# Kernel optimization log

Hardware: AMD Instinct MI355X
Metric: run time of the kernel (lower is better)

Reference implementation:

```python
import jax, jax.numpy as jnp
import numpy as np

D = 1024      # input_dim
H = 16        # head_num
HD = 64       # head_dim
HID = 4096    # mlp hidden
CUR = 512     # cur_seq
PREV = 512    # prev_seq (memory)
FULL = CUR + PREV
BS = 16
SCALE = 1.0 / (HD ** 0.5)


def setup_inputs() -> dict:
    key = jax.random.key(0)
    ks = jax.random.split(key, 20)
    def nrm(k, shape, s=0.02):
        return (jax.random.normal(k, shape) * s).astype(jnp.float32)
    inp = {
        "inputs": nrm(ks[0], (CUR, BS, D), 1.0),
        "pos_embedding": nrm(ks[1], (FULL, 1, D), 1.0),
        "u": nrm(ks[2], (H, HD)),
        "v": nrm(ks[3], (H, HD)),
        "memory": nrm(ks[4], (PREV, BS, D), 1.0),
        # causal mask: position i (query) may attend to j <= i + PREV; True = masked
        "mask": jnp.triu(jnp.ones((CUR, FULL), dtype=bool), k=PREV + 1)[:, :, None],
        # attention params (stored as (in, out); torch Linear applies x @ W.T + b)
        "Wkv": nrm(ks[5], (D, 2 * H * HD)), "bkv": jnp.zeros((2 * H * HD,), jnp.float32),
        "Wq": nrm(ks[6], (D, H * HD)), "bq": jnp.zeros((H * HD,), jnp.float32),
        "Wo": nrm(ks[7], (H * HD, D)), "bo": jnp.zeros((D,), jnp.float32),
        "Wp": nrm(ks[8], (D, H * HD)), "bp": jnp.zeros((H * HD,), jnp.float32),
        # layernorms
        "ln1_g": jnp.ones((D,), jnp.float32), "ln1_b": jnp.zeros((D,), jnp.float32),
        "ln2_g": jnp.ones((D,), jnp.float32), "ln2_b": jnp.zeros((D,), jnp.float32),
        # mlp (mlp_num=2): Linear(D,HID)+relu, Linear(HID,D)+relu
        "W1": nrm(ks[9], (D, HID)), "b1": jnp.zeros((HID,), jnp.float32),
        "W2": nrm(ks[10], (HID, D)), "b2": jnp.zeros((D,), jnp.float32),
        # GRU gates: stacked [Wr,Wz,Wg] and [Ur,Uz,Ug], no bias; bg init 2.0
        "g1_W": nrm(ks[11], (3, D, D)), "g1_U": nrm(ks[12], (3, D, D)),
        "g1_bg": jnp.full((D,), 2.0, jnp.float32),
        "g2_W": nrm(ks[13], (3, D, D)), "g2_U": nrm(ks[14], (3, D, D)),
        "g2_bg": jnp.full((D,), 2.0, jnp.float32),
    }
    return inp


def _layernorm(x, g, b, eps=1e-5):
    mu = jnp.mean(x, axis=-1, keepdims=True)
    var = jnp.mean(jnp.square(x - mu), axis=-1, keepdims=True)
    return (x - mu) * jax.lax.rsqrt(var + eps) * g + b


def _rel_shift(x):
    # x: (bs, head, cur, full) -> pad/reshape/slice trick of Transformer-XL
    b, h, c, f = x.shape
    xp = jnp.pad(x, ((0, 0), (0, 0), (0, 0), (1, 0)))      # (b,h,c,f+1)
    xp = xp.reshape(b, h, f + 1, c)
    return xp[:, :, 1:, :].reshape(b, h, c, f)


def _gru_gate(x, y, W, U, bg):
    # W, U: (3, D, D) for [r, z, g] gates; torch Linear => y @ W[i].T
    r = jax.nn.sigmoid(y @ W[0].T + x @ U[0].T)
    z = jax.nn.sigmoid(y @ W[1].T + x @ U[1].T - bg)
    h = jnp.tanh(y @ W[2].T + (r * x) @ U[2].T)
    return (1.0 - z) * x + z * h


def _attention_xl(x_cur, pos_emb, x_full, u, v, mask,
                  Wkv, bkv, Wq, bq, Wo, bo, Wp, bp):
    cur, bs, _ = x_cur.shape
    full = x_full.shape[0]
    kv = x_full @ Wkv + bkv                                  # (full, bs, 2*H*HD)
    key, value = jnp.split(kv, 2, axis=-1)
    query = x_cur @ Wq + bq                                  # (cur, bs, H*HD)
    r = (pos_emb @ Wp + bp).reshape(full, H, HD)             # (full, H, HD)

    key = key.reshape(full, bs, H, HD)
    value = value.reshape(full, bs, H, HD)
    query = query.reshape(cur, bs, H, HD)

    content = jnp.einsum('ibhd,jbhd->bhij', query + u, key)  # (bs,H,cur,full)
    position = jnp.einsum('ibhd,jhd->bhij', query + v, r)    # (bs,H,cur,full)
    position = _rel_shift(position)

    attn = (content + position) * SCALE
    # mask: (cur, full, 1) bool, True = masked
    m = mask[:, :, 0][None, None]                            # (1,1,cur,full)
    attn = jnp.where(m, -jnp.inf, attn)
    p = jax.nn.softmax(attn, axis=-1)

    out = jnp.einsum('bhij,jbhd->ibhd', p, value).reshape(cur, bs, H * HD)
    return out @ Wo + bo                                     # (cur, bs, D)


def reference(inputs, pos_embedding, u, v, memory, mask,
              Wkv, bkv, Wq, bq, Wo, bo, Wp, bp,
              ln1_g, ln1_b, ln2_g, ln2_b,
              W1, b1, W2, b2,
              g1_W, g1_U, g1_bg, g2_W, g2_U, g2_bg):
    prev = memory.shape[0]
    full_input = jnp.concatenate([memory, inputs], axis=0)   # (full, bs, D)
    x1 = _layernorm(full_input, ln1_g, ln1_b)
    a1 = _attention_xl(x1[prev:], pos_embedding, x1, u, v, mask,
                       Wkv, bkv, Wq, bq, Wo, bo, Wp, bp)
    a1 = jax.nn.relu(a1)                                     # dropout = identity (eval)
    o1 = _gru_gate(inputs, a1, g1_W, g1_U, g1_bg)
    x2 = _layernorm(o1, ln2_g, ln2_b)
    m2 = jax.nn.relu(jax.nn.relu(x2 @ W1 + b1) @ W2 + b2)    # mlp: act after every linear
    o2 = _gru_gate(o1, m2, g2_W, g2_U, g2_bg)
    return o2
```

## Files before the change

### kernel.cpp

```cpp
#include <hip/hip_runtime.h>
#include <stdint.h>

typedef _Float16 h16;
typedef __attribute__((ext_vector_type(8))) _Float16 f16x8;
typedef __attribute__((ext_vector_type(4))) _Float16 f16x4;
typedef __attribute__((ext_vector_type(4))) float f32x4;

enum { F_OBF = 1, F_BIAS = 2, F_RELU = 4, F_ACC = 8 };

#define BARRIER_MEM                                  \
  do {                                               \
    asm volatile("" ::: "memory");                   \
    __builtin_amdgcn_s_barrier();                    \
    asm volatile("" ::: "memory");                   \
  } while (0)

static __device__ __forceinline__ void gload16(const void* g, void* l) {
  __builtin_amdgcn_global_load_lds((__attribute__((address_space(1))) void*)g,
                                   (__attribute__((address_space(3))) void*)l,
                                   16, 0, 0);
}

template <int BN, int FLAGS>
__global__ __launch_bounds__(512) void gemm2_k(
    const h16* __restrict__ A, const h16* __restrict__ B,
    void* __restrict__ Cv, const float* __restrict__ bias,
    int K, int lda, int ldb, int ldc, int gm) {
  constexpr int NH = BN / 128;
  constexpr int WN = BN / 4;
  __shared__ h16 Al[2][256][64];
  __shared__ h16 Bl[2][BN][64];

  const int tid = threadIdx.x, lane = tid & 63, wid = tid >> 6;
  const int wr = wid >> 2, wn = wid & 3;
  const int ar = lane & 15, q4 = lane >> 4;

  const int nwg = gridDim.x, cpx = nwg >> 3;
  const int bid = (blockIdx.x & 7) * cpx + (blockIdx.x >> 3);
  const int mx = bid % gm, ny = bid / gm;

  const h16* Ab = A + (long)mx * 256 * lda;
  const h16* Bb = B + (long)ny * BN * ldb;

  auto stageA = [&](int buf, int half, int k0) {
#pragma unroll
    for (int l = 0; l < 2; ++l) {
      const int idx = l * 512 + tid;
      const int row = half * 128 + (idx >> 3), sl = idx & 7;
      gload16(Ab + (long)row * lda + k0 + (sl ^ (row & 7)) * 8,
              (char*)&Al[buf][0][0] + (half * 1024 + l * 512 + wid * 64) * 16);
    }
  };
  auto stageB = [&](int buf, int half, int k0) {
#pragma unroll
    for (int l = 0; l < NH; ++l) {
      const int idx = l * 512 + tid;
      const int row = half * (BN / 2) + (idx >> 3), sl = idx & 7;
      gload16(Bb + (long)row * ldb + k0 + (sl ^ (row & 7)) * 8,
              (char*)&Bl[buf][0][0] + (half * (BN * 4) + l * 512 + wid * 64) * 16);
    }
  };

  f32x4 acc[8][2 * NH] = {};
  const int nk = K >> 6;

  stageB(0, 0, 0); stageB(0, 1, 0); stageA(0, 0, 0); stageA(0, 1, 0);
  if (nk > 1) { stageB(1, 0, 64); stageB(1, 1, 64); stageA(1, 0, 64); stageA(1, 1, 64); }
  if (nk > 1) {
    if constexpr (NH == 2) asm volatile("s_waitcnt vmcnt(8)" ::: "memory");
    else                   asm volatile("s_waitcnt vmcnt(6)" ::: "memory");
  } else {
    asm volatile("s_waitcnt vmcnt(0)" ::: "memory");
  }
  BARRIER_MEM;

  for (int kt = 0; kt < nk; ++kt) {
    const int b = kt & 1;
    const int k2 = (kt + 2) << 6;
    const bool pf = (kt + 2) < nk;

    f16x8 a0[4][2], b0[NH][2];
#pragma unroll
    for (int m = 0; m < 4; ++m) {
      const int row = wr * 128 + m * 16 + ar;
#pragma unroll
      for (int ks = 0; ks < 2; ++ks)
        a0[m][ks] = *(const f16x8*)&Al[b][row][((ks * 4 + q4) ^ (row & 7)) * 8];
    }
#pragma unroll
    for (int n = 0; n < NH; ++n) {
      const int row = wn * WN + n * 16 + ar;
#pragma unroll
      for (int ks = 0; ks < 2; ++ks)
        b0[n][ks] = *(const f16x8*)&Bl[b][row][((ks * 4 + q4) ^ (row & 7)) * 8];
    }
    BARRIER_MEM;
    __builtin_amdgcn_s_setprio(1);
#pragma unroll
    for (int m = 0; m < 4; ++m)
#pragma unroll
      for (int n = 0; n < NH; ++n)
#pragma unroll
        for (int ks = 0; ks < 2; ++ks)
          acc[m][n] = __builtin_amdgcn_mfma_f32_16x16x32_f16(a0[m][ks], b0[n][ks], acc[m][n], 0, 0, 0);
    __builtin_amdgcn_s_setprio(0);
    BARRIER_MEM;

    f16x8 b1f[NH][2];
#pragma unroll
    for (int n = 0; n < NH; ++n) {
      const int row = wn * WN + (n + NH) * 16 + ar;
#pragma unroll
      for (int ks = 0; ks < 2; ++ks)
        b1f[n][ks] = *(const f16x8*)&Bl[b][row][((ks * 4 + q4) ^ (row & 7)) * 8];
    }
    BARRIER_MEM;
    __builtin_amdgcn_s_setprio(1);
#pragma unroll
    for (int m = 0; m < 4; ++m)
#pragma unroll
      for (int n = 0; n < NH; ++n)
#pragma unroll
        for (int ks = 0; ks < 2; ++ks)
          acc[m][n + NH] = __builtin_amdgcn_mfma_f32_16x16x32_f16(a0[m][ks], b1f[n][ks], acc[m][n + NH], 0, 0, 0);
    __builtin_amdgcn_s_setprio(0);
    BARRIER_MEM;

    f16x8 a1f[4][2];
#pragma unroll
    for (int m = 0; m < 4; ++m) {
      const int row = wr * 128 + (m + 4) * 16 + ar;
#pragma unroll
      for (int ks = 0; ks < 2; ++ks)
        a1f[m][ks] = *(const f16x8*)&Al[b][row][((ks * 4 + q4) ^ (row & 7)) * 8];
    }
    if (pf) { stageB(b, 0, k2); stageB(b, 1, k2); }
    BARRIER_MEM;
    __builtin_amdgcn_s_setprio(1);
#pragma unroll
    for (int m = 0; m < 4; ++m)
#pragma unroll
      for (int n = 0; n < NH; ++n)
#pragma unroll
        for (int ks = 0; ks < 2; ++ks)
          acc[m + 4][n] = __builtin_amdgcn_mfma_f32_16x16x32_f16(a1f[m][ks], b0[n][ks], acc[m + 4][n], 0, 0, 0);
    __builtin_amdgcn_s_setprio(0);
    BARRIER_MEM;

    if (pf) { stageA(b, 0, k2); stageA(b, 1, k2); }
    __builtin_amdgcn_s_setprio(1);
#pragma unroll
    for (int m = 0; m < 4; ++m)
#pragma unroll
      for (int n = 0; n < NH; ++n)
#pragma unroll
        for (int ks = 0; ks < 2; ++ks)
          acc[m + 4][n + NH] = __builtin_amdgcn_mfma_f32_16x16x32_f16(a1f[m][ks], b1f[n][ks], acc[m + 4][n + NH], 0, 0, 0);
    __builtin_amdgcn_s_setprio(0);
    if (pf) {
      if constexpr (NH == 2) asm volatile("s_waitcnt vmcnt(8)" ::: "memory");
      else                   asm volatile("s_waitcnt vmcnt(6)" ::: "memory");
    } else if (kt + 1 < nk) {
      asm volatile("s_waitcnt vmcnt(0)" ::: "memory");
    }
    BARRIER_MEM;
  }

#pragma unroll
  for (int m = 0; m < 8; ++m) {
#pragma unroll
    for (int n = 0; n < 2 * NH; ++n) {
      const int col = ny * BN + wn * WN + n * 16 + ar;
      float bv1 = 0.f;
      if (FLAGS & F_BIAS) bv1 = bias[col];
#pragma unroll
      for (int r = 0; r < 4; ++r) {
        const int row = mx * 256 + wr * 128 + m * 16 + q4 * 4 + r;
        float val = acc[m][n][r] + bv1;
        if (FLAGS & F_RELU) val = fmaxf(val, 0.f);
        if constexpr ((FLAGS & F_ACC) != 0) {
          float* p = (float*)Cv + (long)row * ldc + col;
          *p = *p + val;
        } else if constexpr ((FLAGS & F_OBF) != 0) {
          ((h16*)Cv)[(long)row * ldc + col] = (h16)val;
        } else {
          ((float*)Cv)[(long)row * ldc + col] = val;
        }
      }
    }
  }
}

__global__ __launch_bounds__(256) void fattn_k(
    const h16* __restrict__ qu, const h16* __restrict__ qv,
    const h16* __restrict__ kvb, const h16* __restrict__ vT,
    const h16* __restrict__ rb, h16* __restrict__ attn) {
  __shared__ h16 Kl[2][128][64];
  __shared__ h16 Vl[64][128];
  __shared__ h16 Psc[4][16][164];

  const int tid = threadIdx.x, lane = tid & 63, wv = tid >> 6;
  const int z = blockIdx.x, b = z >> 4, h = z & 15;
  const int i0 = blockIdx.y * 64;
  const int ar = lane & 15, q4 = lane >> 4;
  const int myrow = i0 + wv * 16;
  const h16* vTz = vT + (long)z * 64 * 1024;

  const long qoff = ((long)(myrow + ar) * 16 + b) * 1024 + h * 64 + q4 * 8;
  f16x8 quf[2], qvf[2];
  quf[0] = *(const f16x8*)&qu[qoff];
  quf[1] = *(const f16x8*)&qu[qoff + 32];
  qvf[0] = *(const f16x8*)&qv[qoff];
  qvf[1] = *(const f16x8*)&qv[qoff + 32];

  f32x4 o[4] = {};
  float mrow[4], lrow[4];
#pragma unroll
  for (int r = 0; r < 4; ++r) { mrow[r] = -3e38f; lrow[r] = 0.f; }

  const int ntiles = (i0 + 575 + 128) >> 7;

  auto stageK = [&](int buf, int j0) {
#pragma unroll
    for (int it = 0; it < 4; ++it) {
      const int ch = it * 256 + wv * 64 + lane;
      const int kr = ch >> 3, ks = ch & 7;
      gload16(kvb + ((long)(j0 + kr) * 16 + b) * 2048 + h * 64 + (ks ^ (kr & 7)) * 8,
              (char*)&Kl[buf][0][0] + (it * 256 + wv * 64) * 16);
    }
  };
  auto stageV = [&](int j0) {
#pragma unroll
    for (int it = 0; it < 4; ++it) {
      const int ch = it * 256 + wv * 64 + lane;
      const int vd = ch >> 4, vs = ch & 15;
      gload16(vTz + (long)vd * 1024 + j0 + (vs ^ (vd & 7)) * 8,
              (char*)&Vl[0][0] + (it * 256 + wv * 64) * 16);
    }
  };

  stageK(0, 0);
  asm volatile("s_waitcnt vmcnt(0)" ::: "memory");
  __builtin_amdgcn_s_barrier();

  for (int t = 0; t < ntiles; ++t) {
    const int j0 = t * 128;
    const int kb = t & 1;
    const bool pk = (t + 1) < ntiles;

    stageV(j0);
    if (pk) stageK(kb ^ 1, (t + 1) * 128);
    if (pk) asm volatile("s_waitcnt vmcnt(8)" ::: "memory");
    else    asm volatile("s_waitcnt vmcnt(4)" ::: "memory");
    BARRIER_MEM;

    f32x4 acc_c[8] = {};
#pragma unroll
    for (int kd = 0; kd < 2; ++kd)
#pragma unroll
      for (int nf = 0; nf < 8; ++nf) {
        const int j = nf * 16 + ar;
        const int phys = (kd * 4 + q4) ^ (j & 7);
        const f16x8 kf = *(const f16x8*)&Kl[kb][j][phys * 8];
        acc_c[nf] = __builtin_amdgcn_mfma_f32_16x16x32_f16(quf[kd], kf, acc_c[nf], 0, 0, 0);
      }

    const int jbase = j0 - myrow + 496;
    f32x4 acc_p[9] = {};
#pragma unroll
    for (int kd = 0; kd < 2; ++kd)
#pragma unroll
      for (int jf = 0; jf < 9; ++jf) {
        int jjr = jbase + jf * 16 + ar;
        if (jjr > 1023) jjr = 1023;
        const f16x8 rf = *(const f16x8*)&rb[(long)jjr * 1024 + h * 64 + kd * 32 + q4 * 8];
        acc_p[jf] = __builtin_amdgcn_mfma_f32_16x16x32_f16(qvf[kd], rf, acc_p[jf], 0, 0, 0);
      }
#pragma unroll
    for (int jf = 0; jf < 9; ++jf)
#pragma unroll
      for (int r = 0; r < 4; ++r)
        Psc[wv][q4 * 4 + r][jf * 16 + ar] = (h16)acc_p[jf][r];

    float p[8][4];
#pragma unroll
    for (int nf = 0; nf < 8; ++nf)
#pragma unroll
      for (int r = 0; r < 4; ++r) {
        const int iloc = q4 * 4 + r;
        const int jloc = nf * 16 + ar;
        const int band = jloc - iloc + 15;
        const float pv = (float)Psc[wv][iloc][band];
        float sv = (acc_c[nf][r] + pv) * 0.125f;
        const bool ok = (j0 + jloc) <= (myrow + iloc + 512);
        p[nf][r] = ok ? sv : -3e38f;
      }
#pragma unroll
    for (int r = 0; r < 4; ++r) {
      float tm = -3e38f;
#pragma unroll
      for (int nf = 0; nf < 8; ++nf) tm = fmaxf(tm, p[nf][r]);
      tm = fmaxf(tm, __shfl_xor(tm, 1));
      tm = fmaxf(tm, __shfl_xor(tm, 2));
      tm = fmaxf(tm, __shfl_xor(tm, 4));
      tm = fmaxf(tm, __shfl_xor(tm, 8));
      const float mn = fmaxf(mrow[r], tm);
      const float sc = __expf(mrow[r] - mn);
      mrow[r] = mn;
      float ts = 0.f;
#pragma unroll
      for (int nf = 0; nf < 8; ++nf) {
        const float e = __expf(p[nf][r] - mn);
        p[nf][r] = e;
        ts += e;
      }
      ts += __shfl_xor(ts, 1);
      ts += __shfl_xor(ts, 2);
      ts += __shfl_xor(ts, 4);
      ts += __shfl_xor(ts, 8);
      lrow[r] = lrow[r] * sc + ts;
#pragma unroll
      for (int v = 0; v < 4; ++v) o[v][r] *= sc;
    }

#pragma unroll
    for (int nf = 0; nf < 8; ++nf)
#pragma unroll
      for (int r = 0; r < 4; ++r) {
        const int iloc = q4 * 4 + r, jloc = nf * 16 + ar;
        Psc[wv][iloc][((jloc >> 3) ^ (iloc & 7)) * 8 + (jloc & 7)] = (h16)p[nf][r];
      }

    if (pk) asm volatile("s_waitcnt vmcnt(4)" ::: "memory");
    else    asm volatile("s_waitcnt vmcnt(0)" ::: "memory");
    BARRIER_MEM;

#pragma unroll
    for (int ks = 0; ks < 4; ++ks) {
      const f16x8 pa = *(const f16x8*)&Psc[wv][ar][((ks * 4 + q4) ^ (ar & 7)) * 8];
#pragma unroll
      for (int vnf = 0; vnf < 4; ++vnf) {
        const int d = vnf * 16 + ar;
        const f16x8 vb = *(const f16x8*)&Vl[d][((ks * 4 + q4) ^ (d & 7)) * 8];
        o[vnf] = __builtin_amdgcn_mfma_f32_16x16x32_f16(pa, vb, o[vnf], 0, 0, 0);
      }
    }
    BARRIER_MEM;
  }

#pragma unroll
  for (int vnf = 0; vnf < 4; ++vnf)
#pragma unroll
    for (int r = 0; r < 4; ++r) {
      const int i_ = myrow + q4 * 4 + r;
      attn[((long)i_ * 16 + b) * 1024 + h * 64 + vnf * 16 + ar] =
          (h16)(o[vnf][r] / lrow[r]);
    }
}

__global__ __launch_bounds__(256) void wtrans_k(const float* __restrict__ in,
                                                h16* __restrict__ out, int K, int N) {
  __shared__ float t[32][33];
  const int tx = threadIdx.x & 31, ty = threadIdx.x >> 5;
  const int n0 = blockIdx.x * 32, k0 = blockIdx.y * 32;
#pragma unroll
  for (int j = 0; j < 32; j += 8)
    t[ty + j][tx] = in[(long)(k0 + ty + j) * N + n0 + tx];
  __syncthreads();
#pragma unroll
  for (int j = 0; j < 32; j += 8)
    out[(long)(n0 + ty + j) * K + k0 + tx] = (h16)t[tx][ty + j];
}

__global__ __launch_bounds__(256) void cast_k(const float* __restrict__ in,
                                              h16* __restrict__ out, long n4) {
  const long i = (long)blockIdx.x * 256 + threadIdx.x;
  if (i >= n4) return;
  const float4 v = ((const float4*)in)[i];
  f16x4 o;
  o[0] = (h16)v.x; o[1] = (h16)v.y; o[2] = (h16)v.z; o[3] = (h16)v.w;
  ((f16x4*)out)[i] = o;
}

__global__ __launch_bounds__(256) void cast4_k(
    const float* __restrict__ a, const float* __restrict__ b,
    const float* __restrict__ c, const float* __restrict__ d,
    h16* __restrict__ oa, h16* __restrict__ ob,
    h16* __restrict__ oc, h16* __restrict__ od, long n4) {
  const long i = (long)blockIdx.x * 256 + threadIdx.x;
  if (i >= n4) return;
  const float* in = (blockIdx.y == 0) ? a : (blockIdx.y == 1) ? b : (blockIdx.y == 2) ? c : d;
  h16* out = (blockIdx.y == 0) ? oa : (blockIdx.y == 1) ? ob : (blockIdx.y == 2) ? oc : od;
  const float4 v = ((const float4*)in)[i];
  f16x4 o;
  o[0] = (h16)v.x; o[1] = (h16)v.y; o[2] = (h16)v.z; o[3] = (h16)v.w;
  ((f16x4*)out)[i] = o;
}

__global__ void addbias_k(const float* __restrict__ bq, const float* __restrict__ u,
                          const float* __restrict__ v, float* __restrict__ qu,
                          float* __restrict__ qv) {
  const int c = blockIdx.x * 256 + threadIdx.x;
  if (c < 1024) { qu[c] = bq[c] + u[c]; qv[c] = bq[c] + v[c]; }
}

__global__ __launch_bounds__(256) void zero_out_k(float* __restrict__ out, long n) {
  const long i = (long)blockIdx.x * 256 + threadIdx.x;
  if (i < n) out[i] = 0.f;
}

__global__ __launch_bounds__(256) void ln_k(const float* __restrict__ src0,
                                            const float* __restrict__ src1, int rows0,
                                            const float* __restrict__ g,
                                            const float* __restrict__ b,
                                            h16* __restrict__ out) {
  const int row = blockIdx.x, tid = threadIdx.x;
  const float* src = (row < rows0) ? (src0 + (long)row * 1024)
                                   : (src1 + (long)(row - rows0) * 1024);
  const float4 x = ((const float4*)src)[tid];
  float s = x.x + x.y + x.z + x.w;
  float sq = x.x * x.x + x.y * x.y + x.z * x.z + x.w * x.w;
#pragma unroll
  for (int o = 32; o > 0; o >>= 1) { s += __shfl_down(s, o); sq += __shfl_down(sq, o); }
  __shared__ float red[8];
  const int lane = tid & 63, w = tid >> 6;
  if (lane == 0) { red[w] = s; red[4 + w] = sq; }
  __syncthreads();
  s = red[0] + red[1] + red[2] + red[3];
  sq = red[4] + red[5] + red[6] + red[7];
  const float mu = s * (1.f / 1024.f);
  const float inv = rsqrtf(sq * (1.f / 1024.f) - mu * mu + 1e-5f);
  const float4 gg = ((const float4*)g)[tid], bb = ((const float4*)b)[tid];
  f16x4 o;
  o[0] = (h16)((x.x - mu) * inv * gg.x + bb.x);
  o[1] = (h16)((x.y - mu) * inv * gg.y + bb.y);
  o[2] = (h16)((x.z - mu) * inv * gg.z + bb.z);
  o[3] = (h16)((x.w - mu) * inv * gg.w + bb.w);
  ((f16x4*)(out + (long)row * 1024))[tid] = o;
}

__global__ __launch_bounds__(256) void vtrans_k(const h16* __restrict__ kv,
                                                h16* __restrict__ vT) {
  const int z = blockIdx.y, b = z >> 4, h = z & 15;
  const int j0 = blockIdx.x * 64;
  __shared__ h16 t[64][72];
  const int jj = threadIdx.x >> 3, c = threadIdx.x & 7;
#pragma unroll
  for (int half = 0; half < 2; ++half) {
    const int j = jj + half * 32;
    const f16x8 v = *(const f16x8*)(kv + ((long)(j0 + j) * 16 + b) * 2048 + 1024 + h * 64 + c * 8);
    *(f16x8*)&t[j][c * 8] = v;
  }
  __syncthreads();
#pragma unroll
  for (int half = 0; half < 2; ++half) {
    const int d = jj + half * 32;
    f16x8 o;
#pragma unroll
    for (int k = 0; k < 8; ++k) o[k] = t[c * 8 + k][d];
    *(f16x8*)(vT + ((long)z * 64 + d) * 1024 + j0 + c * 8) = o;
  }
}

__global__ __launch_bounds__(256) void gru_rx_k(const float* __restrict__ T,
                                                const float* __restrict__ x,
                                                h16* __restrict__ rx) {
  const long i = (long)blockIdx.x * 256 + threadIdx.x;
  const long row = i >> 8;
  const int c4 = (int)(i & 255);
  const float4 t = *((const float4*)(T + row * 3072) + c4);
  const float4 xx = ((const float4*)x)[i];
  f16x4 o;
  o[0] = (h16)(xx.x / (1.f + __expf(-t.x)));
  o[1] = (h16)(xx.y / (1.f + __expf(-t.y)));
  o[2] = (h16)(xx.z / (1.f + __expf(-t.z)));
  o[3] = (h16)(xx.w / (1.f + __expf(-t.w)));
  ((f16x4*)rx)[i] = o;
}

__global__ __launch_bounds__(256) void gru_out_k(const float* __restrict__ T,
                                                 const float* __restrict__ x,
                                                 const float* __restrict__ bg,
                                                 float* __restrict__ outf,
                                                 h16* __restrict__ outh) {
  const long i = (long)blockIdx.x * 256 + threadIdx.x;
  const long row = i >> 8;
  const int c4 = (int)(i & 255);
  const float4 tz = *((const float4*)(T + row * 3072 + 1024) + c4);
  const float4 th = *((const float4*)(T + row * 3072 + 2048) + c4);
  const float4 xx = ((const float4*)x)[i];
  const float4 bb = ((const float4*)bg)[c4];
  float4 o;
  {
    const float z0 = 1.f / (1.f + __expf(-(tz.x - bb.x)));
    const float z1 = 1.f / (1.f + __expf(-(tz.y - bb.y)));
    const float z2 = 1.f / (1.f + __expf(-(tz.z - bb.z)));
    const float z3 = 1.f / (1.f + __expf(-(tz.w - bb.w)));
    o.x = (1.f - z0) * xx.x + z0 * tanhf(th.x);
    o.y = (1.f - z1) * xx.y + z1 * tanhf(th.y);
    o.z = (1.f - z2) * xx.z + z2 * tanhf(th.z);
    o.w = (1.f - z3) * xx.w + z3 * tanhf(th.w);
  }
  ((float4*)outf)[i] = o;
  if (outh != nullptr) {
    f16x4 oh;
    oh[0] = (h16)o.x; oh[1] = (h16)o.y; oh[2] = (h16)o.z; oh[3] = (h16)o.w;
    ((f16x4*)outh)[i] = oh;
  }
}

extern "C" void kernel_launch(void* const* d_in, const int* in_sizes, int n_in,
                              void* d_out, int out_size, void* d_ws, size_t ws_size,
                              hipStream_t stream) {
  const float* inputs = (const float*)d_in[0];
  const float* pos    = (const float*)d_in[1];
  const float* u      = (const float*)d_in[2];
  const float* v      = (const float*)d_in[3];
  const float* memory = (const float*)d_in[4];
  const float* Wkv = (const float*)d_in[6];  const float* bkv = (const float*)d_in[7];
  const float* Wq  = (const float*)d_in[8];  const float* bq  = (const float*)d_in[9];
  const float* Wo  = (const float*)d_in[10]; const float* bo  = (const float*)d_in[11];
  const float* Wp  = (const float*)d_in[12]; const float* bp  = (const float*)d_in[13];
  const float* ln1_g = (const float*)d_in[14]; const float* ln1_b = (const float*)d_in[15];
  const float* ln2_g = (const float*)d_in[16]; const float* ln2_b = (const float*)d_in[17];
  const float* W1 = (const float*)d_in[18]; const float* b1 = (const float*)d_in[19];
  const float* W2 = (const float*)d_in[20]; const float* b2 = (const float*)d_in[21];
  const float* g1_W = (const float*)d_in[22]; const float* g1_U = (const float*)d_in[23];
  const float* g1_bg = (const float*)d_in[24];
  const float* g2_W = (const float*)d_in[25]; const float* g2_U = (const float*)d_in[26];
  const float* g2_bg = (const float*)d_in[27];
  (void)in_sizes; (void)n_in;

  const size_t MB = 1u << 20;
  const size_t NEEDED = 247 * MB;
  const dim3 blk(256);
  if (ws_size < NEEDED) {
    zero_out_k<<<(out_size + 255) / 256, blk, 0, stream>>>((float*)d_out, out_size);
    return;
  }

  char* w = (char*)d_ws;
  h16* WoT   = (h16*)(w + 0 * MB);
  h16* W1T   = (h16*)(w + 2 * MB);
  h16* W2T   = (h16*)(w + 10 * MB);
  h16* g1Wb  = (h16*)(w + 18 * MB);
  h16* g1Ub  = (h16*)(w + 24 * MB);
  h16* g2Wb  = (h16*)(w + 30 * MB);
  h16* g2Ub  = (h16*)(w + 36 * MB);
  h16* WkvT  = (h16*)(w + 42 * MB);
  h16* WqT   = (h16*)(w + 46 * MB);
  h16* WpT   = (h16*)(w + 48 * MB);
  h16* posb  = (h16*)(w + 50 * MB);
  float* bias_qu = (float*)(w + 52 * MB);
  float* bias_qv = (float*)(w + 52 * MB + 8192);
  h16* xb    = (h16*)(w + 53 * MB);
  h16* x1    = (h16*)(w + 69 * MB);
  char* Rbig =        w + 101 * MB;
  h16* qu    = (h16*)(w + 197 * MB);
  h16* qv    = (h16*)(w + 213 * MB);
  h16* rb    = (h16*)(w + 229 * MB);
  h16* attn  = (h16*)(w + 231 * MB);

  h16*   kvb  = (h16*)Rbig;
  float* Tall = (float*)Rbig;
  h16*   h1   = (h16*)Rbig;
  h16*   vT   = x1;
  h16*   a1   = qu;
  h16*   rx1  = qv;
  float* o1f  = (float*)qu;
  h16*   o1b  = attn;
  h16*   x2   = x1;
  h16*   m2   = x1 + 8L * 1024 * 1024;
  h16*   rx2  = x1;

  wtrans_k<<<dim3(64, 32), blk, 0, stream>>>(Wkv, WkvT, 1024, 2048);
  wtrans_k<<<dim3(32, 32), blk, 0, stream>>>(Wq, WqT, 1024, 1024);
  wtrans_k<<<dim3(32, 32), blk, 0, stream>>>(Wo, WoT, 1024, 1024);
  wtrans_k<<<dim3(32, 32), blk, 0, stream>>>(Wp, WpT, 1024, 1024);
  wtrans_k<<<dim3(128, 32), blk, 0, stream>>>(W1, W1T, 1024, 4096);
  wtrans_k<<<dim3(32, 128), blk, 0, stream>>>(W2, W2T, 4096, 1024);
  cast4_k<<<dim3(3072, 4), blk, 0, stream>>>(g1_W, g1_U, g2_W, g2_U,
                                             g1Wb, g1Ub, g2Wb, g2Ub, 786432);
  cast_k<<<1024, blk, 0, stream>>>(pos, posb, 262144);
  cast_k<<<8192, blk, 0, stream>>>(inputs, xb, 2097152);
  addbias_k<<<4, blk, 0, stream>>>(bq, u, v, bias_qu, bias_qv);

  ln_k<<<16384, blk, 0, stream>>>(memory, inputs, 8192, ln1_g, ln1_b, x1);

  gemm2_k<256, F_OBF | F_BIAS><<<dim3(512), dim3(512), 0, stream>>>(
      x1, WkvT, kvb, bkv, 1024, 1024, 1024, 2048, 64);
  gemm2_k<128, F_OBF | F_BIAS><<<dim3(256), dim3(512), 0, stream>>>(
      x1 + 8192L * 1024, WqT, qu, bias_qu, 1024, 1024, 1024, 1024, 32);
  gemm2_k<128, F_OBF | F_BIAS><<<dim3(256), dim3(512), 0, stream>>>(
      x1 + 8192L * 1024, WqT, qv, bias_qv, 1024, 1024, 1024, 1024, 32);
  gemm2_k<128, F_OBF | F_BIAS><<<dim3(32), dim3(512), 0, stream>>>(
      posb, WpT, rb, bp, 1024, 1024, 1024, 1024, 4);
  vtrans_k<<<dim3(16, 256), blk, 0, stream>>>(kvb, vT);

  fattn_k<<<dim3(256, 8), blk, 0, stream>>>(qu, qv, kvb, vT, rb, attn);

  gemm2_k<128, F_OBF | F_BIAS | F_RELU><<<dim3(256), dim3(512), 0, stream>>>(
      attn, WoT, a1, bo, 1024, 1024, 1024, 1024, 32);

  gemm2_k<256, 0><<<dim3(384), dim3(512), 0, stream>>>(
      a1, g1Wb, Tall, nullptr, 1024, 1024, 1024, 3072, 32);
  gemm2_k<256, F_ACC><<<dim3(256), dim3(512), 0, stream>>>(
      xb, g1Ub, Tall, nullptr, 1024, 1024, 1024, 3072, 32);
  gru_rx_k<<<8192, blk, 0, stream>>>(Tall, inputs, rx1);
  gemm2_k<128, F_ACC><<<dim3(256), dim3(512), 0, stream>>>(
      rx1, g1Ub + 2L * 1024 * 1024, Tall + 2048, nullptr, 1024, 1024, 1024, 3072, 32);
  gru_out_k<<<8192, blk, 0, stream>>>(Tall, inputs, g1_bg, o1f, o1b);

  ln_k<<<8192, blk, 0, stream>>>(o1f, o1f, 8192, ln2_g, ln2_b, x2);
  gemm2_k<256, F_OBF | F_BIAS | F_RELU><<<dim3(512), dim3(512), 0, stream>>>(
      x2, W1T, h1, b1, 1024, 1024, 1024, 4096, 32);
  gemm2_k<128, F_OBF | F_BIAS | F_RELU><<<dim3(256), dim3(512), 0, stream>>>(
      h1, W2T, m2, b2, 4096, 4096, 4096, 1024, 32);

  gemm2_k<256, 0><<<dim3(384), dim3(512), 0, stream>>>(
      m2, g2Wb, Tall, nullptr, 1024, 1024, 1024, 3072, 32);
  gemm2_k<256, F_ACC><<<dim3(256), dim3(512), 0, stream>>>(
      o1b, g2Ub, Tall, nullptr, 1024, 1024, 1024, 3072, 32);
  gru_rx_k<<<8192, blk, 0, stream>>>(Tall, o1f, rx2);
  gemm2_k<128, F_ACC><<<dim3(256), dim3(512), 0, stream>>>(
      rx2, g2Ub + 2L * 1024 * 1024, Tall + 2048, nullptr, 1024, 1024, 1024, 3072, 32);
  gru_out_k<<<8192, blk, 0, stream>>>(Tall, o1f, g2_bg, (float*)d_out, nullptr);
}
```

Before: 1.118 ms.

## Fuse qu/qv projections and restructure attention relative-position shift via shuffles

The two query GEMMs that differ only in bias are merged into one GEMM with a dual-output epilogue, so the activation and weight traffic for Wq is read once. In the attention kernel, the relative-shift band extraction now goes through cross-lane shuffles instead of a shared-memory round trip. The K tile drops to a single buffer with a rescheduled barrier/prefetch order, and positional-embedding loads are issued early. Single-buffering K shrinks LDS use but serialises some K loads against compute, and the added shuffles raise register pressure.

```diff
diff --git a/kernel.cpp b/kernel.cpp
--- a/kernel.cpp
+++ b/kernel.cpp
@@ -6,7 +6,7 @@
 typedef __attribute__((ext_vector_type(4))) _Float16 f16x4;
 typedef __attribute__((ext_vector_type(4))) float f32x4;
 
-enum { F_OBF = 1, F_BIAS = 2, F_RELU = 4, F_ACC = 8 };
+enum { F_OBF = 1, F_BIAS = 2, F_RELU = 4, F_ACC = 8, F_DUAL = 16 };
 
 #define BARRIER_MEM                                  \
   do {                                               \
@@ -25,7 +25,8 @@
 __global__ __launch_bounds__(512) void gemm2_k(
     const h16* __restrict__ A, const h16* __restrict__ B,
     void* __restrict__ Cv, const float* __restrict__ bias,
-    int K, int lda, int ldb, int ldc, int gm) {
+    int K, int lda, int ldb, int ldc, int gm,
+    void* __restrict__ C2v, const float* __restrict__ bias2) {
   constexpr int NH = BN / 128;
   constexpr int WN = BN / 4;
   __shared__ h16 Al[2][256][64];
@@ -171,8 +172,9 @@
 #pragma unroll
     for (int n = 0; n < 2 * NH; ++n) {
       const int col = ny * BN + wn * WN + n * 16 + ar;
-      float bv1 = 0.f;
+      float bv1 = 0.f, bv2 = 0.f;
       if (FLAGS & F_BIAS) bv1 = bias[col];
+      if (FLAGS & F_DUAL) bv2 = bias2[col];
 #pragma unroll
       for (int r = 0; r < 4; ++r) {
         const int row = mx * 256 + wr * 128 + m * 16 + q4 * 4 + r;
@@ -183,6 +185,8 @@
           *p = *p + val;
         } else if constexpr ((FLAGS & F_OBF) != 0) {
           ((h16*)Cv)[(long)row * ldc + col] = (h16)val;
+          if constexpr ((FLAGS & F_DUAL) != 0)
+            ((h16*)C2v)[(long)row * ldc + col] = (h16)(acc[m][n][r] + bv2);
         } else {
           ((float*)Cv)[(long)row * ldc + col] = val;
         }
@@ -191,13 +195,13 @@
   }
 }
 
-__global__ __launch_bounds__(256) void fattn_k(
+__global__ __launch_bounds__(256, 1) void fattn_k(
     const h16* __restrict__ qu, const h16* __restrict__ qv,
     const h16* __restrict__ kvb, const h16* __restrict__ vT,
     const h16* __restrict__ rb, h16* __restrict__ attn) {
-  __shared__ h16 Kl[2][128][64];
+  __shared__ h16 Kl[128][64];
   __shared__ h16 Vl[64][128];
-  __shared__ h16 Psc[4][16][164];
+  __shared__ h16 Psc[4][16][128];
 
   const int tid = threadIdx.x, lane = tid & 63, wv = tid >> 6;
   const int z = blockIdx.x, b = z >> 4, h = z & 15;
@@ -220,13 +224,13 @@
 
   const int ntiles = (i0 + 575 + 128) >> 7;
 
-  auto stageK = [&](int buf, int j0) {
+  auto stageK = [&](int j0) {
 #pragma unroll
     for (int it = 0; it < 4; ++it) {
       const int ch = it * 256 + wv * 64 + lane;
       const int kr = ch >> 3, ks = ch & 7;
       gload16(kvb + ((long)(j0 + kr) * 16 + b) * 2048 + h * 64 + (ks ^ (kr & 7)) * 8,
-              (char*)&Kl[buf][0][0] + (it * 256 + wv * 64) * 16);
+              (char*)&Kl[0][0] + (it * 256 + wv * 64) * 16);
     }
   };
   auto stageV = [&](int j0) {
@@ -239,20 +243,23 @@
     }
   };
 
-  stageK(0, 0);
-  asm volatile("s_waitcnt vmcnt(0)" ::: "memory");
-  __builtin_amdgcn_s_barrier();
+  stageK(0);
 
   for (int t = 0; t < ntiles; ++t) {
     const int j0 = t * 128;
-    const int kb = t & 1;
     const bool pk = (t + 1) < ntiles;
 
-    stageV(j0);
-    if (pk) stageK(kb ^ 1, (t + 1) * 128);
-    if (pk) asm volatile("s_waitcnt vmcnt(8)" ::: "memory");
-    else    asm volatile("s_waitcnt vmcnt(4)" ::: "memory");
-    BARRIER_MEM;
+    asm volatile("s_waitcnt vmcnt(0)" ::: "memory");
+    BARRIER_MEM;
+
+    const int jbase = j0 - myrow + 496;
+    f16x8 rf0[9];
+#pragma unroll
+    for (int jf = 0; jf < 9; ++jf) {
+      int jjr = jbase + jf * 16 + ar;
+      if (jjr > 1023) jjr = 1023;
+      rf0[jf] = *(const f16x8*)&rb[(long)jjr * 1024 + h * 64 + q4 * 8];
+    }
 
     f32x4 acc_c[8] = {};
 #pragma unroll
@@ -261,40 +268,47 @@
       for (int nf = 0; nf < 8; ++nf) {
         const int j = nf * 16 + ar;
         const int phys = (kd * 4 + q4) ^ (j & 7);
-        const f16x8 kf = *(const f16x8*)&Kl[kb][j][phys * 8];
+        const f16x8 kf = *(const f16x8*)&Kl[j][phys * 8];
         acc_c[nf] = __builtin_amdgcn_mfma_f32_16x16x32_f16(quf[kd], kf, acc_c[nf], 0, 0, 0);
       }
-
-    const int jbase = j0 - myrow + 496;
+    BARRIER_MEM;
+
+    f16x8 rf1[9];
+#pragma unroll
+    for (int jf = 0; jf < 9; ++jf) {
+      int jjr = jbase + jf * 16 + ar;
+      if (jjr > 1023) jjr = 1023;
+      rf1[jf] = *(const f16x8*)&rb[(long)jjr * 1024 + h * 64 + 32 + q4 * 8];
+    }
+    stageV(j0);
+    if (pk) stageK((t + 1) * 128);
+
     f32x4 acc_p[9] = {};
 #pragma unroll
-    for (int kd = 0; kd < 2; ++kd)
-#pragma unroll
-      for (int jf = 0; jf < 9; ++jf) {
-        int jjr = jbase + jf * 16 + ar;
-        if (jjr > 1023) jjr = 1023;
-        const f16x8 rf = *(const f16x8*)&rb[(long)jjr * 1024 + h * 64 + kd * 32 + q4 * 8];
-        acc_p[jf] = __builtin_amdgcn_mfma_f32_16x16x32_f16(qvf[kd], rf, acc_p[jf], 0, 0, 0);
+    for (int jf = 0; jf < 9; ++jf)
+      acc_p[jf] = __builtin_amdgcn_mfma_f32_16x16x32_f16(qvf[0], rf0[jf], acc_p[jf], 0, 0, 0);
+#pragma unroll
+    for (int jf = 0; jf < 9; ++jf)
+      acc_p[jf] = __builtin_amdgcn_mfma_f32_16x16x32_f16(qvf[1], rf1[jf], acc_p[jf], 0, 0, 0);
+
+    float p[8][4];
+#pragma unroll
+    for (int r = 0; r < 4; ++r) {
+      const int iloc = q4 * 4 + r;
+      const int src = q4 * 16 + ((ar - iloc + 15) & 15);
+      float g[9];
+#pragma unroll
+      for (int jf = 0; jf < 9; ++jf) g[jf] = __shfl(acc_p[jf][r], src, 64);
+      const bool hi = ar > iloc;
+      const int lim = myrow + iloc + 512 - j0;
+#pragma unroll
+      for (int nf = 0; nf < 8; ++nf) {
+        const float pv = hi ? g[nf + 1] : g[nf];
+        const float sv = (acc_c[nf][r] + pv) * 0.125f;
+        p[nf][r] = (nf * 16 + ar <= lim) ? sv : -3e38f;
       }
-#pragma unroll
-    for (int jf = 0; jf < 9; ++jf)
-#pragma unroll
-      for (int r = 0; r < 4; ++r)
-        Psc[wv][q4 * 4 + r][jf * 16 + ar] = (h16)acc_p[jf][r];
-
-    float p[8][4];
-#pragma unroll
-    for (int nf = 0; nf < 8; ++nf)
-#pragma unroll
-      for (int r = 0; r < 4; ++r) {
-        const int iloc = q4 * 4 + r;
-        const int jloc = nf * 16 + ar;
-        const int band = jloc - iloc + 15;
-        const float pv = (float)Psc[wv][iloc][band];
-        float sv = (acc_c[nf][r] + pv) * 0.125f;
-        const bool ok = (j0 + jloc) <= (myrow + iloc + 512);
-        p[nf][r] = ok ? sv : -3e38f;
-      }
+    }
+
 #pragma unroll
     for (int r = 0; r < 4; ++r) {
       float tm = -3e38f;
@@ -345,7 +359,6 @@
         o[vnf] = __builtin_amdgcn_mfma_f32_16x16x32_f16(pa, vb, o[vnf], 0, 0, 0);
       }
     }
-    BARRIER_MEM;
   }
 
 #pragma unroll
@@ -588,41 +601,41 @@
   ln_k<<<16384, blk, 0, stream>>>(memory, inputs, 8192, ln1_g, ln1_b, x1);
 
   gemm2_k<256, F_OBF | F_BIAS><<<dim3(512), dim3(512), 0, stream>>>(
-      x1, WkvT, kvb, bkv, 1024, 1024, 1024, 2048, 64);
-  gemm2_k<128, F_OBF | F_BIAS><<<dim3(256), dim3(512), 0, stream>>>(
-      x1 + 8192L * 1024, WqT, qu, bias_qu, 1024, 1024, 1024, 1024, 32);
-  gemm2_k<128, F_OBF | F_BIAS><<<dim3(256), dim3(512), 0, stream>>>(
-      x1 + 8192L * 1024, WqT, qv, bias_qv, 1024, 1024, 1024, 1024, 32);
+      x1, WkvT, kvb, bkv, 1024, 1024, 1024, 2048, 64, nullptr, nullptr);
+  gemm2_k<128, F_OBF | F_BIAS | F_DUAL><<<dim3(256), dim3(512), 0, stream>>>(
+      x1 + 8192L * 1024, WqT, qu, bias_qu, 1024, 1024, 1024, 1024, 32, qv, bias_qv);
   gemm2_k<128, F_OBF | F_BIAS><<<dim3(32), dim3(512), 0, stream>>>(
-      posb, WpT, rb, bp, 1024, 1024, 1024, 1024, 4);
+      posb, WpT, rb, bp, 1024, 1024, 1024, 1024, 4, nullptr, nullptr);
   vtrans_k<<<dim3(16, 256), blk, 0, stream>>>(kvb, vT);
 
   fattn_k<<<dim3(256, 8), blk, 0, stream>>>(qu, qv, kvb, vT, rb, attn);
 
   gemm2_k<128, F_OBF | F_BIAS | F_RELU><<<dim3(256), dim3(512), 0, stream>>>(
-      attn, WoT, a1, bo, 1024, 1024, 1024, 1024, 32);
+      attn, WoT, a1, bo, 1024, 1024, 1024, 1024, 32, nullptr, nullptr);
 
   gemm2_k<256, 0><<<dim3(384), dim3(512), 0, stream>>>(
-      a1, g1Wb, Tall, nullptr, 1024, 1024, 1024, 3072, 32);
+      a1, g1Wb, Tall, nullptr, 1024, 1024, 1024, 3072, 32, nullptr, nullptr);
   gemm2_k<256, F_ACC><<<dim3(256), dim3(512), 0, stream>>>(
-      xb, g1Ub, Tall, nullptr, 1024, 1024, 1024, 3072, 32);
+      xb, g1Ub, Tall, nullptr, 1024, 1024, 1024, 3072, 32, nullptr, nullptr);
   gru_rx_k<<<8192, blk, 0, stream>>>(Tall, inputs, rx1);
   gemm2_k<128, F_ACC><<<dim3(256), dim3(512), 0, stream>>>(
-      rx1, g1Ub + 2L * 1024 * 1024, Tall + 2048, nullptr, 1024, 1024, 1024, 3072, 32);
+      rx1, g1Ub + 2L * 1024 * 1024, Tall + 2048, nullptr, 1024, 1024, 1024, 3072, 32,
+      nullptr, nullptr);
   gru_out_k<<<8192, blk, 0, stream>>>(Tall, inputs, g1_bg, o1f, o1b);
 
   ln_k<<<8192, blk, 0, stream>>>(o1f, o1f, 8192, ln2_g, ln2_b, x2);
   gemm2_k<256, F_OBF | F_BIAS | F_RELU><<<dim3(512), dim3(512), 0, stream>>>(
-      x2, W1T, h1, b1, 1024, 1024, 1024, 4096, 32);
+      x2, W1T, h1, b1, 1024, 1024, 1024, 4096, 32, nullptr, nullptr);
   gemm2_k<128, F_OBF | F_BIAS | F_RELU><<<dim3(256), dim3(512), 0, stream>>>(
-      h1, W2T, m2, b2, 4096, 4096, 4096, 1024, 32);
+      h1, W2T, m2, b2, 4096, 4096, 4096, 1024, 32, nullptr, nullptr);
 
   gemm2_k<256, 0><<<dim3(384), dim3(512), 0, stream>>>(
-      m2, g2Wb, Tall, nullptr, 1024, 1024, 1024, 3072, 32);
+      m2, g2Wb, Tall, nullptr, 1024, 1024, 1024, 3072, 32, nullptr, nullptr);
   gemm2_k<256, F_ACC><<<dim3(256), dim3(512), 0, stream>>>(
-      o1b, g2Ub, Tall, nullptr, 1024, 1024, 1024, 3072, 32);
+      o1b, g2Ub, Tall, nullptr, 1024, 1024, 1024, 3072, 32, nullptr, nullptr);
   gru_rx_k<<<8192, blk, 0, stream>>>(Tall, o1f, rx2);
   gemm2_k<128, F_ACC><<<dim3(256), dim3(512), 0, stream>>>(
-      rx2, g2Ub + 2L * 1024 * 1024, Tall + 2048, nullptr, 1024, 1024, 1024, 3072, 32);
+      rx2, g2Ub + 2L * 1024 * 1024, Tall + 2048, nullptr, 1024, 1024, 1024, 3072, 32,
+      nullptr, nullptr);
   gru_out_k<<<8192, blk, 0, stream>>>(Tall, o1f, g2_bg, (float*)d_out, nullptr);
 }
```

Measured after the change: 1.215 ms. 8.7% more time.

## Concatenate GRU W/U weights into K=2048 GEMMs and fuse dual Q projections

Applied to the files above, without the earlier changes.

Packs each GRU gate's W and U matrices side by side into one K=2048 weight, and writes the activation and the gate input interleaved into a [y|x] buffer. Each gate stage then runs as a single longer-K GEMM instead of separate GEMMs plus read-modify-write accumulation into an fp32 buffer. The two Q projections (with u and v biases) now share one GEMM that writes two outputs. This removes redundant launches, accumulation traffic and a repeated Q GEMM, at the cost of a more intricate buffer layout and aliasing.

```diff
diff --git a/kernel.cpp b/kernel.cpp
--- a/kernel.cpp
+++ b/kernel.cpp
@@ -6,7 +6,7 @@
 typedef __attribute__((ext_vector_type(4))) _Float16 f16x4;
 typedef __attribute__((ext_vector_type(4))) float f32x4;
 
-enum { F_OBF = 1, F_BIAS = 2, F_RELU = 4, F_ACC = 8 };
+enum { F_OBF = 1, F_BIAS = 2, F_RELU = 4, F_ACC = 8, F_DUAL = 16 };
 
 #define BARRIER_MEM                                  \
   do {                                               \
@@ -25,7 +25,8 @@
 __global__ __launch_bounds__(512) void gemm2_k(
     const h16* __restrict__ A, const h16* __restrict__ B,
     void* __restrict__ Cv, const float* __restrict__ bias,
-    int K, int lda, int ldb, int ldc, int gm) {
+    int K, int lda, int ldb, int ldc, int gm,
+    void* __restrict__ C2v, const float* __restrict__ bias2) {
   constexpr int NH = BN / 128;
   constexpr int WN = BN / 4;
   __shared__ h16 Al[2][256][64];
@@ -171,8 +172,9 @@
 #pragma unroll
     for (int n = 0; n < 2 * NH; ++n) {
       const int col = ny * BN + wn * WN + n * 16 + ar;
-      float bv1 = 0.f;
+      float bv1 = 0.f, bv2 = 0.f;
       if (FLAGS & F_BIAS) bv1 = bias[col];
+      if (FLAGS & F_DUAL) bv2 = bias2[col];
 #pragma unroll
       for (int r = 0; r < 4; ++r) {
         const int row = mx * 256 + wr * 128 + m * 16 + q4 * 4 + r;
@@ -183,6 +185,8 @@
           *p = *p + val;
         } else if constexpr ((FLAGS & F_OBF) != 0) {
           ((h16*)Cv)[(long)row * ldc + col] = (h16)val;
+          if constexpr ((FLAGS & F_DUAL) != 0)
+            ((h16*)C2v)[(long)row * ldc + col] = (h16)(acc[m][n][r] + bv2);
         } else {
           ((float*)Cv)[(long)row * ldc + col] = val;
         }
@@ -382,19 +386,36 @@
   ((f16x4*)out)[i] = o;
 }
 
-__global__ __launch_bounds__(256) void cast4_k(
-    const float* __restrict__ a, const float* __restrict__ b,
-    const float* __restrict__ c, const float* __restrict__ d,
-    h16* __restrict__ oa, h16* __restrict__ ob,
-    h16* __restrict__ oc, h16* __restrict__ od, long n4) {
+__global__ __launch_bounds__(256) void gateprep_k(
+    const float* __restrict__ W1g, const float* __restrict__ U1g,
+    const float* __restrict__ W2g, const float* __restrict__ U2g,
+    h16* __restrict__ o1, h16* __restrict__ o2) {
   const long i = (long)blockIdx.x * 256 + threadIdx.x;
-  if (i >= n4) return;
-  const float* in = (blockIdx.y == 0) ? a : (blockIdx.y == 1) ? b : (blockIdx.y == 2) ? c : d;
-  h16* out = (blockIdx.y == 0) ? oa : (blockIdx.y == 1) ? ob : (blockIdx.y == 2) ? oc : od;
+  const long elem = i * 4;
+  const int row = (int)(elem >> 11);
+  const int col = (int)(elem & 2047);
+  const int gate = row >> 10, oc = row & 1023;
+  const float* W = (blockIdx.y == 0) ? W1g : W2g;
+  const float* U = (blockIdx.y == 0) ? U1g : U2g;
+  h16* out = (blockIdx.y == 0) ? o1 : o2;
+  const float* src = (col < 1024)
+      ? (W + (long)gate * 1048576 + (long)oc * 1024 + col)
+      : (U + (long)gate * 1048576 + (long)oc * 1024 + (col - 1024));
+  const float4 v = *(const float4*)src;
+  f16x4 o;
+  o[0] = (h16)v.x; o[1] = (h16)v.y; o[2] = (h16)v.z; o[3] = (h16)v.w;
+  *(f16x4*)(out + elem) = o;
+}
+
+__global__ __launch_bounds__(256) void xcast_k(const float* __restrict__ in,
+                                               h16* __restrict__ yx) {
+  const long i = (long)blockIdx.x * 256 + threadIdx.x;
+  const long row = i >> 8;
+  const int c4 = (int)(i & 255);
   const float4 v = ((const float4*)in)[i];
   f16x4 o;
   o[0] = (h16)v.x; o[1] = (h16)v.y; o[2] = (h16)v.z; o[3] = (h16)v.w;
-  ((f16x4*)out)[i] = o;
+  *(f16x4*)(yx + row * 2048 + 1024 + c4 * 4) = o;
 }
 
 __global__ void addbias_k(const float* __restrict__ bq, const float* __restrict__ u,
@@ -464,21 +485,22 @@
 
 __global__ __launch_bounds__(256) void gru_rx_k(const float* __restrict__ T,
                                                 const float* __restrict__ x,
-                                                h16* __restrict__ rx) {
+                                                h16* __restrict__ yx) {
   const long i = (long)blockIdx.x * 256 + threadIdx.x;
   const long row = i >> 8;
   const int c4 = (int)(i & 255);
-  const float4 t = *((const float4*)(T + row * 3072) + c4);
+  const float4 t = *((const float4*)(T + row * 2048) + c4);
   const float4 xx = ((const float4*)x)[i];
   f16x4 o;
   o[0] = (h16)(xx.x / (1.f + __expf(-t.x)));
   o[1] = (h16)(xx.y / (1.f + __expf(-t.y)));
   o[2] = (h16)(xx.z / (1.f + __expf(-t.z)));
   o[3] = (h16)(xx.w / (1.f + __expf(-t.w)));
-  ((f16x4*)rx)[i] = o;
+  *(f16x4*)(yx + row * 2048 + 1024 + c4 * 4) = o;
 }
 
 __global__ __launch_bounds__(256) void gru_out_k(const float* __restrict__ T,
+                                                 const float* __restrict__ G,
                                                  const float* __restrict__ x,
                                                  const float* __restrict__ bg,
                                                  float* __restrict__ outf,
@@ -486,8 +508,8 @@
   const long i = (long)blockIdx.x * 256 + threadIdx.x;
   const long row = i >> 8;
   const int c4 = (int)(i & 255);
-  const float4 tz = *((const float4*)(T + row * 3072 + 1024) + c4);
-  const float4 th = *((const float4*)(T + row * 3072 + 2048) + c4);
+  const float4 tz = *((const float4*)(T + row * 2048 + 1024) + c4);
+  const float4 th = *((const float4*)(G + row * 1024) + c4);
   const float4 xx = ((const float4*)x)[i];
   const float4 bb = ((const float4*)bg)[c4];
   float4 o;
@@ -505,7 +527,7 @@
   if (outh != nullptr) {
     f16x4 oh;
     oh[0] = (h16)o.x; oh[1] = (h16)o.y; oh[2] = (h16)o.z; oh[3] = (h16)o.w;
-    ((f16x4*)outh)[i] = oh;
+    *(f16x4*)(outh + row * 2048 + 1024 + c4 * 4) = oh;
   }
 }
 
@@ -543,35 +565,30 @@
   h16* WoT   = (h16*)(w + 0 * MB);
   h16* W1T   = (h16*)(w + 2 * MB);
   h16* W2T   = (h16*)(w + 10 * MB);
-  h16* g1Wb  = (h16*)(w + 18 * MB);
-  h16* g1Ub  = (h16*)(w + 24 * MB);
-  h16* g2Wb  = (h16*)(w + 30 * MB);
-  h16* g2Ub  = (h16*)(w + 36 * MB);
+  h16* g1B   = (h16*)(w + 18 * MB);
+  h16* g2B   = (h16*)(w + 30 * MB);
   h16* WkvT  = (h16*)(w + 42 * MB);
   h16* WqT   = (h16*)(w + 46 * MB);
   h16* WpT   = (h16*)(w + 48 * MB);
   h16* posb  = (h16*)(w + 50 * MB);
   float* bias_qu = (float*)(w + 52 * MB);
   float* bias_qv = (float*)(w + 52 * MB + 8192);
-  h16* xb    = (h16*)(w + 53 * MB);
-  h16* x1    = (h16*)(w + 69 * MB);
-  char* Rbig =        w + 101 * MB;
-  h16* qu    = (h16*)(w + 197 * MB);
-  h16* qv    = (h16*)(w + 213 * MB);
-  h16* rb    = (h16*)(w + 229 * MB);
-  h16* attn  = (h16*)(w + 231 * MB);
+  h16* yx1   = (h16*)(w + 53 * MB);
+  h16* x1    = (h16*)(w + 85 * MB);
+  char* Rbig =        w + 117 * MB;
+  h16* qu    = (h16*)(w + 181 * MB);
+  h16* qv    = (h16*)(w + 197 * MB);
+  h16* attn  = (h16*)(w + 213 * MB);
+  h16* rb    = (h16*)(w + 245 * MB);
 
   h16*   kvb  = (h16*)Rbig;
-  float* Tall = (float*)Rbig;
+  float* Trz  = (float*)Rbig;
   h16*   h1   = (h16*)Rbig;
+  float* Tg   = (float*)qu;
   h16*   vT   = x1;
-  h16*   a1   = qu;
-  h16*   rx1  = qv;
-  float* o1f  = (float*)qu;
-  h16*   o1b  = attn;
-  h16*   x2   = x1;
-  h16*   m2   = x1 + 8L * 1024 * 1024;
-  h16*   rx2  = x1;
+  h16*   yx2  = x1;
+  float* o1f  = (float*)attn;
+  h16*   x2   = yx1;
 
   wtrans_k<<<dim3(64, 32), blk, 0, stream>>>(Wkv, WkvT, 1024, 2048);
   wtrans_k<<<dim3(32, 32), blk, 0, stream>>>(Wq, WqT, 1024, 1024);
@@ -579,50 +596,43 @@
   wtrans_k<<<dim3(32, 32), blk, 0, stream>>>(Wp, WpT, 1024, 1024);
   wtrans_k<<<dim3(128, 32), blk, 0, stream>>>(W1, W1T, 1024, 4096);
   wtrans_k<<<dim3(32, 128), blk, 0, stream>>>(W2, W2T, 4096, 1024);
-  cast4_k<<<dim3(3072, 4), blk, 0, stream>>>(g1_W, g1_U, g2_W, g2_U,
-                                             g1Wb, g1Ub, g2Wb, g2Ub, 786432);
+  gateprep_k<<<dim3(6144, 2), blk, 0, stream>>>(g1_W, g1_U, g2_W, g2_U, g1B, g2B);
   cast_k<<<1024, blk, 0, stream>>>(pos, posb, 262144);
-  cast_k<<<8192, blk, 0, stream>>>(inputs, xb, 2097152);
+  xcast_k<<<8192, blk, 0, stream>>>(inputs, yx1);
   addbias_k<<<4, blk, 0, stream>>>(bq, u, v, bias_qu, bias_qv);
 
   ln_k<<<16384, blk, 0, stream>>>(memory, inputs, 8192, ln1_g, ln1_b, x1);
 
   gemm2_k<256, F_OBF | F_BIAS><<<dim3(512), dim3(512), 0, stream>>>(
-      x1, WkvT, kvb, bkv, 1024, 1024, 1024, 2048, 64);
-  gemm2_k<128, F_OBF | F_BIAS><<<dim3(256), dim3(512), 0, stream>>>(
-      x1 + 8192L * 1024, WqT, qu, bias_qu, 1024, 1024, 1024, 1024, 32);
-  gemm2_k<128, F_OBF | F_BIAS><<<dim3(256), dim3(512), 0, stream>>>(
-      x1 + 8192L * 1024, WqT, qv, bias_qv, 1024, 1024, 1024, 1024, 32);
+      x1, WkvT, kvb, bkv, 1024, 1024, 1024, 2048, 64, nullptr, nullptr);
+  gemm2_k<128, F_OBF | F_BIAS | F_DUAL><<<dim3(256), dim3(512), 0, stream>>>(
+      x1 + 8192L * 1024, WqT, qu, bias_qu, 1024, 1024, 1024, 1024, 32, qv, bias_qv);
   gemm2_k<128, F_OBF | F_BIAS><<<dim3(32), dim3(512), 0, stream>>>(
-      posb, WpT, rb, bp, 1024, 1024, 1024, 1024, 4);
+      posb, WpT, rb, bp, 1024, 1024, 1024, 1024, 4, nullptr, nullptr);
   vtrans_k<<<dim3(16, 256), blk, 0, stream>>>(kvb, vT);
 
   fattn_k<<<dim3(256, 8), blk, 0, stream>>>(qu, qv, kvb, vT, rb, attn);
 
   gemm2_k<128, F_OBF | F_BIAS | F_RELU><<<dim3(256), dim3(512), 0, stream>>>(
-      attn, WoT, a1, bo, 1024, 1024, 1024, 1024, 32);
-
-  gemm2_k<256, 0><<<dim3(384), dim3(512), 0, stream>>>(
-      a1, g1Wb, Tall, nullptr, 1024, 1024, 1024, 3072, 32);
-  gemm2_k<256, F_ACC><<<dim3(256), dim3(512), 0, stream>>>(
-      xb, g1Ub, Tall, nullptr, 1024, 1024, 1024, 3072, 32);
-  gru_rx_k<<<8192, blk, 0, stream>>>(Tall, inputs, rx1);
-  gemm2_k<128, F_ACC><<<dim3(256), dim3(512), 0, stream>>>(
-      rx1, g1Ub + 2L * 1024 * 1024, Tall + 2048, nullptr, 1024, 1024, 1024, 3072, 32);
-  gru_out_k<<<8192, blk, 0, stream>>>(Tall, inputs, g1_bg, o1f, o1b);
+      attn, WoT, yx1, bo, 1024, 1024, 1024, 2048, 32, nullptr, nullptr);
+
+  gemm2_k<256, 0><<<dim3(256), dim3(512), 0, stream>>>(
+      yx1, g1B, Trz, nullptr, 2048, 2048, 2048, 2048, 32, nullptr, nullptr);
+  gru_rx_k<<<8192, blk, 0, stream>>>(Trz, inputs, yx1);
+  gemm2_k<128, 0><<<dim3(256), dim3(512), 0, stream>>>(
+      yx1, g1B + 2048L * 2048, Tg, nullptr, 2048, 2048, 2048, 1024, 32, nullptr, nullptr);
+  gru_out_k<<<8192, blk, 0, stream>>>(Trz, Tg, inputs, g1_bg, o1f, yx2);
 
   ln_k<<<8192, blk, 0, stream>>>(o1f, o1f, 8192, ln2_g, ln2_b, x2);
   gemm2_k<256, F_OBF | F_BIAS | F_RELU><<<dim3(512), dim3(512), 0, stream>>>(
-      x2, W1T, h1, b1, 1024, 1024, 1024, 4096, 32);
+      x2, W1T, h1, b1, 1024, 1024, 1024, 4096, 32, nullptr, nullptr);
   gemm2_k<128, F_OBF | F_BIAS | F_RELU><<<dim3(256), dim3(512), 0, stream>>>(
-      h1, W2T, m2, b2, 4096, 4096, 4096, 1024, 32);
-
-  gemm2_k<256, 0><<<dim3(384), dim3(512), 0, stream>>>(
-      m2, g2Wb, Tall, nullptr, 1024, 1024, 1024, 3072, 32);
-  gemm2_k<256, F_ACC><<<dim3(256), dim3(512), 0, stream>>>(
-      o1b, g2Ub, Tall, nullptr, 1024, 1024, 1024, 3072, 32);
-  gru_rx_k<<<8192, blk, 0, stream>>>(Tall, o1f, rx2);
-  gemm2_k<128, F_ACC><<<dim3(256), dim3(512), 0, stream>>>(
-      rx2, g2Ub + 2L * 1024 * 1024, Tall + 2048, nullptr, 1024, 1024, 1024, 3072, 32);
-  gru_out_k<<<8192, blk, 0, stream>>>(Tall, o1f, g2_bg, (float*)d_out, nullptr);
-}
+      h1, W2T, yx2, b2, 4096, 4096, 4096, 2048, 32, nullptr, nullptr);
+
+  gemm2_k<256, 0><<<dim3(256), dim3(512), 0, stream>>>(
+      yx2, g2B, Trz, nullptr, 2048, 2048, 2048, 2048, 32, nullptr, nullptr);
+  gru_rx_k<<<8192, blk, 0, stream>>>(Trz, o1f, yx2);
+  gemm2_k<128, 0><<<dim3(256), dim3(512), 0, stream>>>(
+      yx2, g2B + 2048L * 2048, Tg, nullptr, 2048, 2048, 2048, 1024, 32, nullptr, nullptr);
+  gru_out_k<<<8192, blk, 0, stream>>>(Trz, Tg, o1f, g2_bg, (float*)d_out, nullptr);
+}
```

Result: faster. 1.007 ms (-10.0%).
